# Optimization experiments

Measured on AMD Instinct MI355X. Metric: run time of the kernel, lower is better.

Reference implementation:

```python
import jax, jax.numpy as jnp
import numpy as np
from jax.scipy.special import i0e

BATCH = 64
D1, D2 = 1024, 256
ALPHA = 1.0
BETA = 0.0
WT_3D = 0.95
WT_2D = 0.05

# Score-function moments: per-observation mean/variance of exp(-0.5*A*s)
# for a random direction mismatch on the sphere (3D) / circle (2D).

def score_mean(A):
    # 3D: |z|^2 = 2(1-cos t) uniform on [0,4] -> E = (1 - e^{-2A}) / (2A)
    return (1.0 - jnp.exp(-2.0 * A)) / (2.0 * A)

def score_var(A):
    mean_s2 = (1.0 - jnp.exp(-4.0 * A)) / (4.0 * A)
    return mean_s2 - score_mean(A) ** 2

def score_mean_2d(A):
    # 2D: E[exp(-A(1-cos t))] = e^{-A} I0(A) = i0e(A)
    return i0e(A)

def score_var_2d(A):
    return i0e(2.0 * A) - score_mean_2d(A) ** 2


def setup_inputs() -> dict:
    key = jax.random.key(0)
    k1, k2 = jax.random.split(key)
    # z: difference of predicted vs observed unit direction vectors (small)
    z = jax.random.normal(k1, (BATCH, D1, D2, 3), dtype=jnp.float32) * 0.1
    # R: resolution factor in radians, per orbital element
    R = jax.random.uniform(k2, (BATCH,), dtype=jnp.float32, minval=0.02, maxval=0.1)
    num_obs = 100000  # total number of real (non-padded) observations
    return {"z": z, "R": R, "num_obs": num_obs}


def reference(z, R, num_obs):
    num_obs = jnp.float32(num_obs)
    A = 1.0 / (R * R)                       # [B]
    Bcoef = (-0.5 * A)[:, None, None]       # [B,1,1]
    # NOTE: original code uses norm (NOT squared norm) inside the exponent
    arg = Bcoef * jnp.linalg.norm(z, axis=-1)          # [B, D1, D2]
    raw_score = jnp.sum(jnp.exp(arg), axis=(1, 2))     # [B]
    mu_per_obs = WT_3D * score_mean(A) + WT_2D * score_mean_2d(A)
    mu = num_obs * mu_per_obs                          # [B]
    var_per_obs = WT_3D * score_var(A) + WT_2D * score_var_2d(A)
    sigma2 = num_obs * var_per_obs                     # [B]
    objective = raw_score - ALPHA * mu - BETA * sigma2 # [B]
    return raw_score, mu, sigma2, objective
```

## Files before the change

### kernel.cpp

```cpp
#include <hip/hip_runtime.h>

#define BATCH 64
#define D1 1024
#define D2 256
#define BLOCKS_PER_BATCH 64
#define THREADS 256

__global__ __launch_bounds__(THREADS) void score_sum_kernel(
        const float* __restrict__ z,
        const float* __restrict__ R,
        float* __restrict__ partial) {
    const int b = blockIdx.y;
    const int tid = blockIdx.x * THREADS + threadIdx.x;

    const float Rb = R[b];
    const float Bc = -0.5f / (Rb * Rb);

    const float4* __restrict__ zb =
        (const float4*)(z + (size_t)b * ((size_t)D1 * D2 * 3));

    float acc = 0.0f;
#pragma unroll
    for (int g = 0; g < 4; ++g) {
        const int group = g * 16384 + tid;
        const float4 v0 = zb[group * 3 + 0];
        const float4 v1 = zb[group * 3 + 1];
        const float4 v2 = zb[group * 3 + 2];
        const float n0 = sqrtf(fmaf(v0.x, v0.x, fmaf(v0.y, v0.y, v0.z * v0.z)));
        const float n1 = sqrtf(fmaf(v0.w, v0.w, fmaf(v1.x, v1.x, v1.y * v1.y)));
        const float n2 = sqrtf(fmaf(v1.z, v1.z, fmaf(v1.w, v1.w, v2.x * v2.x)));
        const float n3 = sqrtf(fmaf(v2.y, v2.y, fmaf(v2.z, v2.z, v2.w * v2.w)));
        acc += __expf(Bc * n0) + __expf(Bc * n1) + __expf(Bc * n2) + __expf(Bc * n3);
    }

    const int lane = threadIdx.x & 63;
    const int wave = threadIdx.x >> 6;
    for (int off = 32; off; off >>= 1) acc += __shfl_down(acc, off, 64);

    __shared__ float lds[THREADS / 64];
    if (lane == 0) lds[wave] = acc;
    __syncthreads();
    if (threadIdx.x == 0) {
        float s = lds[0] + lds[1] + lds[2] + lds[3];
        partial[b * BLOCKS_PER_BATCH + blockIdx.x] = s;
    }
}

__device__ inline double i0e_large(double x) {
    const double ix = 1.0 / x;
    const double s = 1.0 + ix * (0.125
                   + ix * (0.0703125
                   + ix * (0.0732421875
                   + ix * (0.112152099609375
                   + ix * 0.22711181640625))));
    return s / sqrt(6.283185307179586476925286766559 * x);
}

__global__ __launch_bounds__(64) void finalize_kernel(
        const float* __restrict__ partial,
        const float* __restrict__ R,
        const int* __restrict__ num_obs_p,
        float* __restrict__ out) {
    const int b = blockIdx.x;
    const int t = threadIdx.x;

    float v = partial[b * BLOCKS_PER_BATCH + t];
    for (int off = 32; off; off >>= 1) v += __shfl_down(v, off, 64);

    if (t == 0) {
        const double nobs = (double)num_obs_p[0];
        const double Rb = (double)R[b];
        const double A = 1.0 / (Rb * Rb);

        const double e2 = exp(-2.0 * A);
        const double e4 = exp(-4.0 * A);
        const double mean3 = (1.0 - e2) / (2.0 * A);
        const double ms2_3 = (1.0 - e4) / (4.0 * A);
        const double var3 = ms2_3 - mean3 * mean3;

        const double i0eA  = i0e_large(A);
        const double i0e2A = i0e_large(2.0 * A);
        const double var2 = i0e2A - i0eA * i0eA;

        const double WT3 = 0.95, WT2 = 0.05;
        const double mu     = nobs * (WT3 * mean3 + WT2 * i0eA);
        const double sigma2 = nobs * (WT3 * var3  + WT2 * var2);
        const double raw    = (double)v;
        const double ALPHA = 1.0, BETA = 0.0;
        const double objective = raw - ALPHA * mu - BETA * sigma2;

        out[b]           = (float)raw;
        out[BATCH + b]   = (float)mu;
        out[2*BATCH + b] = (float)sigma2;
        out[3*BATCH + b] = (float)objective;
    }
}

extern "C" void kernel_launch(void* const* d_in, const int* in_sizes, int n_in,
                              void* d_out, int out_size, void* d_ws, size_t ws_size,
                              hipStream_t stream) {
    const float* z    = (const float*)d_in[0];
    const float* R    = (const float*)d_in[1];
    const int*   nobs = (const int*)d_in[2];
    float* out = (float*)d_out;
    float* partial = (float*)d_ws;

    dim3 grid(BLOCKS_PER_BATCH, BATCH);
    score_sum_kernel<<<grid, THREADS, 0, stream>>>(z, R, partial);
    finalize_kernel<<<BATCH, 64, 0, stream>>>(partial, R, nobs, out);
}
```

Before: 275.3 us.

## Stage z through LDS with register prefetch and halve block count

Replaces the direct strided float4 loads with fully coalesced contiguous segment loads staged into shared memory. Each thread then reads its 12 floats from LDS. The next segment is prefetched into registers while the current one is computed, and each block now handles 8 segments, with blocks per batch halved. This adds two barriers per iteration and an LDS round trip to a kernel that is bound by memory bandwidth, and it lowers the number of blocks in flight.

```diff
diff --git a/kernel.cpp b/kernel.cpp
--- a/kernel.cpp
+++ b/kernel.cpp
@@ -3,46 +3,81 @@
 #define BATCH 64
 #define D1 1024
 #define D2 256
-#define BLOCKS_PER_BATCH 64
+#define BPB 32
 #define THREADS 256
+#define ITERS 8
+#define SEG_F4 (THREADS * 3)
+
 
 __global__ __launch_bounds__(THREADS) void score_sum_kernel(
         const float* __restrict__ z,
         const float* __restrict__ R,
         float* __restrict__ partial) {
     const int b = blockIdx.y;
-    const int tid = blockIdx.x * THREADS + threadIdx.x;
+    const int tid = threadIdx.x;
 
     const float Rb = R[b];
     const float Bc = -0.5f / (Rb * Rb);
 
-    const float4* __restrict__ zb =
-        (const float4*)(z + (size_t)b * ((size_t)D1 * D2 * 3));
+    const float4* __restrict__ zb4 =
+        (const float4*)z + (size_t)b * ((size_t)(D1 * D2 * 3) / 4);
+
+    __shared__ float4 buf[SEG_F4];
+    const float* lds_f = (const float*)buf;
 
     float acc = 0.0f;
-#pragma unroll
-    for (int g = 0; g < 4; ++g) {
-        const int group = g * 16384 + tid;
-        const float4 v0 = zb[group * 3 + 0];
-        const float4 v1 = zb[group * 3 + 1];
-        const float4 v2 = zb[group * 3 + 2];
-        const float n0 = sqrtf(fmaf(v0.x, v0.x, fmaf(v0.y, v0.y, v0.z * v0.z)));
-        const float n1 = sqrtf(fmaf(v0.w, v0.w, fmaf(v1.x, v1.x, v1.y * v1.y)));
-        const float n2 = sqrtf(fmaf(v1.z, v1.z, fmaf(v1.w, v1.w, v2.x * v2.x)));
-        const float n3 = sqrtf(fmaf(v2.y, v2.y, fmaf(v2.z, v2.z, v2.w * v2.w)));
+
+    int seg = blockIdx.x;
+    {
+        const size_t base = (size_t)seg * SEG_F4 + tid;
+        float4 p0 = zb4[base];
+        float4 p1 = zb4[base + THREADS];
+        float4 p2 = zb4[base + 2 * THREADS];
+        buf[tid] = p0;
+        buf[tid + THREADS] = p1;
+        buf[tid + 2 * THREADS] = p2;
+    }
+    __syncthreads();
+
+    for (int it = 0; it < ITERS; ++it) {
+        const bool more = (it + 1 < ITERS);
+        float4 r0, r1, r2;
+        if (more) {
+            const size_t base = (size_t)(seg + BPB) * SEG_F4 + tid;
+            r0 = zb4[base];
+            r1 = zb4[base + THREADS];
+            r2 = zb4[base + 2 * THREADS];
+        }
+
+        const float4* my = (const float4*)(lds_f + 12 * tid);
+        const float4 a = my[0];
+        const float4 c = my[1];
+        const float4 d = my[2];
+        const float n0 = sqrtf(fmaf(a.x, a.x, fmaf(a.y, a.y, a.z * a.z)));
+        const float n1 = sqrtf(fmaf(a.w, a.w, fmaf(c.x, c.x, c.y * c.y)));
+        const float n2 = sqrtf(fmaf(c.z, c.z, fmaf(c.w, c.w, d.x * d.x)));
+        const float n3 = sqrtf(fmaf(d.y, d.y, fmaf(d.z, d.z, d.w * d.w)));
         acc += __expf(Bc * n0) + __expf(Bc * n1) + __expf(Bc * n2) + __expf(Bc * n3);
+
+        __syncthreads();
+        if (more) {
+            buf[tid] = r0;
+            buf[tid + THREADS] = r1;
+            buf[tid + 2 * THREADS] = r2;
+        }
+        __syncthreads();
+        seg += BPB;
     }
 
     const int lane = threadIdx.x & 63;
     const int wave = threadIdx.x >> 6;
     for (int off = 32; off; off >>= 1) acc += __shfl_down(acc, off, 64);
 
-    __shared__ float lds[THREADS / 64];
-    if (lane == 0) lds[wave] = acc;
+    __shared__ float red[THREADS / 64];
+    if (lane == 0) red[wave] = acc;
     __syncthreads();
     if (threadIdx.x == 0) {
-        float s = lds[0] + lds[1] + lds[2] + lds[3];
-        partial[b * BLOCKS_PER_BATCH + blockIdx.x] = s;
+        partial[b * BPB + blockIdx.x] = red[0] + red[1] + red[2] + red[3];
     }
 }
 
@@ -64,7 +99,7 @@
     const int b = blockIdx.x;
     const int t = threadIdx.x;
 
-    float v = partial[b * BLOCKS_PER_BATCH + t];
+    float v = (t < BPB) ? partial[b * BPB + t] : 0.0f;
     for (int off = 32; off; off >>= 1) v += __shfl_down(v, off, 64);
 
     if (t == 0) {
@@ -86,13 +121,12 @@
         const double mu     = nobs * (WT3 * mean3 + WT2 * i0eA);
         const double sigma2 = nobs * (WT3 * var3  + WT2 * var2);
         const double raw    = (double)v;
-        const double ALPHA = 1.0, BETA = 0.0;
-        const double objective = raw - ALPHA * mu - BETA * sigma2;
+        const double objective = raw - mu;
 
-        out[b]           = (float)raw;
-        out[BATCH + b]   = (float)mu;
-        out[2*BATCH + b] = (float)sigma2;
-        out[3*BATCH + b] = (float)objective;
+        out[b]             = (float)raw;
+        out[BATCH + b]     = (float)mu;
+        out[2 * BATCH + b] = (float)sigma2;
+        out[3 * BATCH + b] = (float)objective;
     }
 }
 
@@ -105,7 +139,7 @@
     float* out = (float*)d_out;
     float* partial = (float*)d_ws;
 
-    dim3 grid(BLOCKS_PER_BATCH, BATCH);
+    dim3 grid(BPB, BATCH);
     score_sum_kernel<<<grid, THREADS, 0, stream>>>(z, R, partial);
     finalize_kernel<<<BATCH, 64, 0, stream>>>(partial, R, nobs, out);
 }
```

After: 276.5 us. Within noise of the previous version (+0.4%).
